# Kernel optimization log

Hardware: AMD Instinct MI355X
Metric: run time of the kernel (lower is better)

Reference implementation:

```python
import jax, jax.numpy as jnp
import numpy as np

NU = 60000   # num_users
NI = 40000   # num_items
N = NU + NI  # num_nodes
E = 2000000  # num_edges
F = 128      # feat_dim (user_feat_dim == item_feat_dim)
H = 128      # hidden_dim


def setup_inputs() -> dict:
    key = jax.random.key(0)
    ks = jax.random.split(key, 14)
    s = 0.05
    inp = {
        "x": jax.random.normal(ks[0], (N, F), jnp.float32),
        "edge_index": jax.random.randint(ks[1], (2, E), 0, N, dtype=jnp.int32),
        "node_type": jnp.concatenate([jnp.zeros(NU, jnp.int32), jnp.ones(NI, jnp.int32)]),
        # input projections (Linear stores weight as (out, in))
        "w_user": s * jax.random.normal(ks[2], (H, F), jnp.float32),
        "b_user": jnp.zeros((H,), jnp.float32),
        "w_item": s * jax.random.normal(ks[3], (H, F), jnp.float32),
        "b_item": jnp.zeros((H,), jnp.float32),
        # SAGEConv layer 0: lin_l (aggregated neighbors, with bias), lin_r (root, no bias)
        "w_l0": s * jax.random.normal(ks[4], (H, H), jnp.float32),
        "b_l0": s * jax.random.normal(ks[5], (H,), jnp.float32),
        "w_r0": s * jax.random.normal(ks[6], (H, H), jnp.float32),
        # SAGEConv layer 1
        "w_l1": s * jax.random.normal(ks[7], (H, H), jnp.float32),
        "b_l1": s * jax.random.normal(ks[8], (H,), jnp.float32),
        "w_r1": s * jax.random.normal(ks[9], (H, H), jnp.float32),
    }
    return inp


def _sage_conv(h, src, dst, w_l, b_l, w_r):
    # gather source features, max-aggregate onto destinations (PyG aggr='max')
    msg = h[src]                                          # [E, H]
    agg = jax.ops.segment_max(msg, dst, num_segments=N)   # [N, H], -inf where no in-edges
    agg = jnp.where(jnp.isneginf(agg), 0.0, agg)          # PyG fills empty segments with 0
    return agg @ w_l.T + b_l + h @ w_r.T


def reference(x, edge_index, node_type, w_user, b_user, w_item, b_item,
              w_l0, b_l0, w_r0, w_l1, b_l1, w_r1):
    # node_type is sorted: first NU rows are users, rest are items
    src, dst = edge_index[0], edge_index[1]
    user_h = x[:NU] @ w_user.T + b_user                   # [NU, H]
    item_h = x[NU:] @ w_item.T + b_item                   # [NI, H]
    h = jnp.concatenate([user_h, item_h], axis=0)         # [N, H]
    # layer 0 with residual (dims match) then ReLU; dropout is identity in eval
    h = h + _sage_conv(h, src, dst, w_l0, b_l0, w_r0)
    h = jax.nn.relu(h)
    # layer 1 with residual (no activation after last layer)
    h = h + _sage_conv(h, src, dst, w_l1, b_l1, w_r1)
    return (h[:NU], h[NU:])
```

## Files before the change

kernel.cpp:

```cpp
#include <hip/hip_runtime.h>

#define NUSR 60000
#define NITM 40000
#define NN   100000
#define EE   2000000
#define HD   128
#define NEG_BIG (-3.402823466e+38f)

#define BW   512
#define NB   196
#define EPB  8192

using bf16x8   = __attribute__((ext_vector_type(8))) short;
using f32x4    = __attribute__((ext_vector_type(4))) float;
using ushort4t = __attribute__((ext_vector_type(4))) unsigned short;

__device__ __forceinline__ unsigned short f2bf(float f) {
    unsigned int u = __float_as_uint(f);
    u += 0x7FFFu + ((u >> 16) & 1u);
    return (unsigned short)(u >> 16);
}
__device__ __forceinline__ float bf2f(unsigned short s) {
    return __uint_as_float(((unsigned int)s) << 16);
}
__device__ __forceinline__ int swz(int row, int col) {
    return row * HD + (col ^ ((row & 7) << 3));
}

__global__ __launch_bounds__(256) void bhist_k(const int* __restrict__ dst,
                                               int* __restrict__ bcnt) {
    __shared__ int h[NB];
    int t = threadIdx.x;
    if (t < NB) h[t] = 0;
    __syncthreads();
    int e0 = blockIdx.x * EPB;
    #pragma unroll 4
    for (int i = t; i < EPB; i += 256) {
        int e = e0 + i;
        if (e < EE) atomicAdd(&h[dst[e] >> 9], 1);
    }
    __syncthreads();
    if (t < NB && h[t]) atomicAdd(&bcnt[t], h[t]);
}

__global__ void bscan_k(const int* __restrict__ bcnt, int* __restrict__ bbase,
                        int* __restrict__ bcur, int* __restrict__ off) {
    __shared__ int s[256];
    int t = threadIdx.x;
    int v = (t < NB) ? bcnt[t] : 0;
    s[t] = v;
    __syncthreads();
    for (int d = 1; d < 256; d <<= 1) {
        int a = (t >= d) ? s[t - d] : 0;
        __syncthreads();
        s[t] += a;
        __syncthreads();
    }
    if (t < NB) { bbase[t] = s[t] - v; bcur[t] = s[t] - v; }
    if (t == NB - 1) { bbase[NB] = s[t]; off[NN] = EE; }
}

__global__ __launch_bounds__(256) void bscatter_k(const int* __restrict__ src,
                                                  const int* __restrict__ dst,
                                                  int* __restrict__ bcur,
                                                  uint2* __restrict__ bedge) {
    __shared__ int h[NB], base[NB];
    int t = threadIdx.x;
    if (t < NB) h[t] = 0;
    __syncthreads();
    int e0 = blockIdx.x * EPB;
    #pragma unroll 4
    for (int i = t; i < EPB; i += 256) {
        int e = e0 + i;
        if (e < EE) atomicAdd(&h[dst[e] >> 9], 1);
    }
    __syncthreads();
    if (t < NB) {
        int c = h[t];
        base[t] = c ? atomicAdd(&bcur[t], c) : 0;
        h[t] = 0;
    }
    __syncthreads();
    #pragma unroll 4
    for (int i = t; i < EPB; i += 256) {
        int e = e0 + i;
        if (e < EE) {
            int d = dst[e];
            int b = d >> 9;
            int p = base[b] + atomicAdd(&h[b], 1);
            bedge[p] = make_uint2((unsigned)src[e], (unsigned)d);
        }
    }
}

__global__ __launch_bounds__(512) void bcsr_k(const uint2* __restrict__ bedge,
                                              const int* __restrict__ bbase,
                                              int* __restrict__ off,
                                              int* __restrict__ csr) {
    __shared__ int cnt[BW], cur[BW], sc[BW];
    int b = blockIdx.x, t = threadIdx.x;
    int n0 = b * BW;
    int nloc = min(BW, NN - n0);
    cnt[t] = 0;
    __syncthreads();
    int e0 = bbase[b], e1 = bbase[b + 1];
    for (int e = e0 + t; e < e1; e += 512)
        atomicAdd(&cnt[(int)bedge[e].y - n0], 1);
    __syncthreads();
    int v = cnt[t];
    sc[t] = v;
    __syncthreads();
    for (int d = 1; d < BW; d <<= 1) {
        int a = (t >= d) ? sc[t - d] : 0;
        __syncthreads();
        sc[t] += a;
        __syncthreads();
    }
    int excl = sc[t] - v;
    if (t < nloc) { off[n0 + t] = e0 + excl; cur[t] = e0 + excl; }
    __syncthreads();
    for (int e = e0 + t; e < e1; e += 512) {
        uint2 ed = bedge[e];
        int p = atomicAdd(&cur[(int)ed.y - n0], 1);
        csr[p] = (int)ed.x;
    }
}

__global__ void cvt6_k(const float* __restrict__ a0, const float* __restrict__ a1,
                       const float* __restrict__ a2, const float* __restrict__ a3,
                       const float* __restrict__ a4, const float* __restrict__ a5,
                       unsigned short* __restrict__ out) {
    int i = blockIdx.x * 256 + threadIdx.x;
    const float* s;
    switch (i >> 14) {
        case 0: s = a0; break; case 1: s = a1; break; case 2: s = a2; break;
        case 3: s = a3; break; case 4: s = a4; break; default: s = a5; break;
    }
    out[i] = f2bf(s[i & 16383]);
}

__global__ __launch_bounds__(256) void proj_mfma_k(
    const float* __restrict__ x, const unsigned short* __restrict__ wb,
    const float* __restrict__ bias, unsigned short* __restrict__ hout,
    int row_base, int nrows) {
    __shared__ unsigned short lw[HD * HD];
    int tid = threadIdx.x;
    #pragma unroll
    for (int it = 0; it < 16; ++it) {
        int flat = (it * 256 + tid) * 4;
        int row = flat >> 7, col = flat & 127;
        *(ushort4t*)&lw[swz(row, col)] = *(const ushort4t*)(wb + flat);
    }
    __syncthreads();
    int lane = tid & 63, w = tid >> 6;
    int l15 = lane & 15, l4 = lane >> 4;
    int m0 = blockIdx.x * 128 + w * 32;
    f32x4 acc[2][8] = {};
    #pragma unroll
    for (int kb = 0; kb < 4; ++kb) {
        bf16x8 a[2];
        #pragma unroll
        for (int rt = 0; rt < 2; ++rt) {
            int r = m0 + rt * 16 + l15;
            if (r >= nrows) r = nrows - 1;
            const float* ap = x + (size_t)(row_base + r) * HD + kb * 32 + l4 * 8;
            f32x4 v0 = *(const f32x4*)ap;
            f32x4 v1 = *(const f32x4*)(ap + 4);
            bf16x8 f;
            #pragma unroll
            for (int j = 0; j < 4; ++j) { f[j] = (short)f2bf(v0[j]); f[j + 4] = (short)f2bf(v1[j]); }
            a[rt] = f;
        }
        #pragma unroll
        for (int ct = 0; ct < 8; ++ct) {
            bf16x8 b = *(const bf16x8*)&lw[swz(ct * 16 + l15, kb * 32 + l4 * 8)];
            acc[0][ct] = __builtin_amdgcn_mfma_f32_16x16x32_bf16(a[0], b, acc[0][ct], 0, 0, 0);
            acc[1][ct] = __builtin_amdgcn_mfma_f32_16x16x32_bf16(a[1], b, acc[1][ct], 0, 0, 0);
        }
    }
    #pragma unroll
    for (int ct = 0; ct < 8; ++ct) {
        int col = ct * 16 + l15;
        float bv = bias[col];
        #pragma unroll
        for (int rt = 0; rt < 2; ++rt)
            #pragma unroll
            for (int j = 0; j < 4; ++j) {
                int r = m0 + rt * 16 + l4 * 4 + j;
                if (r < nrows)
                    hout[(size_t)(row_base + r) * HD + col] = f2bf(acc[rt][ct][j] + bv);
            }
    }
}

__global__ __launch_bounds__(256) void agg_bf16_k(
    const unsigned short* __restrict__ hb, const int* __restrict__ off,
    const int* __restrict__ csr, unsigned short* __restrict__ aggb) {
    int node = (blockIdx.x * 256 + threadIdx.x) >> 6;
    int lane = threadIdx.x & 63;
    if (node >= NN) return;
    int s0 = off[node], s1 = off[node + 1];
    const unsigned int* hr = (const unsigned int*)hb;
    float m0 = NEG_BIG, m1 = NEG_BIG;
    int j = s0;
    for (; j + 3 < s1; j += 4) {
        int r0 = csr[j], r1 = csr[j + 1], r2 = csr[j + 2], r3 = csr[j + 3];
        unsigned v0 = hr[(size_t)r0 * 64 + lane];
        unsigned v1 = hr[(size_t)r1 * 64 + lane];
        unsigned v2 = hr[(size_t)r2 * 64 + lane];
        unsigned v3 = hr[(size_t)r3 * 64 + lane];
        m0 = fmaxf(fmaxf(m0, __uint_as_float(v0 << 16)), fmaxf(__uint_as_float(v1 << 16), __uint_as_float(v2 << 16)));
        m1 = fmaxf(fmaxf(m1, __uint_as_float(v0 & 0xFFFF0000u)), fmaxf(__uint_as_float(v1 & 0xFFFF0000u), __uint_as_float(v2 & 0xFFFF0000u)));
        m0 = fmaxf(m0, __uint_as_float(v3 << 16));
        m1 = fmaxf(m1, __uint_as_float(v3 & 0xFFFF0000u));
    }
    for (; j < s1; ++j) {
        unsigned v = hr[(size_t)csr[j] * 64 + lane];
        m0 = fmaxf(m0, __uint_as_float(v << 16));
        m1 = fmaxf(m1, __uint_as_float(v & 0xFFFF0000u));
    }
    unsigned outv = (s1 > s0) ? ((__float_as_uint(m0) >> 16) | (__float_as_uint(m1) & 0xFFFF0000u)) : 0u;
    ((unsigned int*)aggb)[(size_t)node * 64 + lane] = outv;
}

__global__ __launch_bounds__(256) void combine_mfma_k(
    const unsigned short* __restrict__ hb, const unsigned short* __restrict__ aggb,
    const unsigned short* __restrict__ wlb, const float* __restrict__ bl,
    const unsigned short* __restrict__ wrb,
    unsigned short* __restrict__ hnext, float* __restrict__ fout, int relu) {
    __shared__ unsigned short lw[2][HD * HD];
    int tid = threadIdx.x;
    #pragma unroll
    for (int it = 0; it < 16; ++it) {
        int flat = (it * 256 + tid) * 4;
        int row = flat >> 7, col = flat & 127;
        *(ushort4t*)&lw[0][swz(row, col)] = *(const ushort4t*)(wlb + flat);
        *(ushort4t*)&lw[1][swz(row, col)] = *(const ushort4t*)(wrb + flat);
    }
    __syncthreads();
    int lane = tid & 63, w = tid >> 6;
    int l15 = lane & 15, l4 = lane >> 4;
    int m0 = blockIdx.x * 128 + w * 32;
    f32x4 acc[2][8] = {};
    #pragma unroll
    for (int kb = 0; kb < 4; ++kb) {
        bf16x8 a1[2], a2[2];
        #pragma unroll
        for (int rt = 0; rt < 2; ++rt) {
            int r = m0 + rt * 16 + l15;
            if (r >= NN) r = NN - 1;
            size_t o = (size_t)r * HD + kb * 32 + l4 * 8;
            a1[rt] = *(const bf16x8*)(aggb + o);
            a2[rt] = *(const bf16x8*)(hb + o);
        }
        #pragma unroll
        for (int ct = 0; ct < 8; ++ct) {
            bf16x8 b1 = *(const bf16x8*)&lw[0][swz(ct * 16 + l15, kb * 32 + l4 * 8)];
            bf16x8 b2 = *(const bf16x8*)&lw[1][swz(ct * 16 + l15, kb * 32 + l4 * 8)];
            acc[0][ct] = __builtin_amdgcn_mfma_f32_16x16x32_bf16(a1[0], b1, acc[0][ct], 0, 0, 0);
            acc[0][ct] = __builtin_amdgcn_mfma_f32_16x16x32_bf16(a2[0], b2, acc[0][ct], 0, 0, 0);
            acc[1][ct] = __builtin_amdgcn_mfma_f32_16x16x32_bf16(a1[1], b1, acc[1][ct], 0, 0, 0);
            acc[1][ct] = __builtin_amdgcn_mfma_f32_16x16x32_bf16(a2[1], b2, acc[1][ct], 0, 0, 0);
        }
    }
    #pragma unroll
    for (int ct = 0; ct < 8; ++ct) {
        int col = ct * 16 + l15;
        float bv = bl[col];
        #pragma unroll
        for (int rt = 0; rt < 2; ++rt)
            #pragma unroll
            for (int j = 0; j < 4; ++j) {
                int r = m0 + rt * 16 + l4 * 4 + j;
                if (r < NN) {
                    float v = acc[rt][ct][j] + bv + bf2f(hb[(size_t)r * HD + col]);
                    if (relu) v = fmaxf(v, 0.0f);
                    if (fout) fout[(size_t)r * HD + col] = v;
                    else      hnext[(size_t)r * HD + col] = f2bf(v);
                }
            }
    }
}

extern "C" void kernel_launch(void* const* d_in, const int* in_sizes, int n_in,
                              void* d_out, int out_size, void* d_ws, size_t ws_size,
                              hipStream_t stream) {
    const float* x      = (const float*)d_in[0];
    const int*   ei     = (const int*)d_in[1];
    const float* w_user = (const float*)d_in[3];
    const float* b_user = (const float*)d_in[4];
    const float* w_item = (const float*)d_in[5];
    const float* b_item = (const float*)d_in[6];
    const float* w_l0   = (const float*)d_in[7];
    const float* b_l0   = (const float*)d_in[8];
    const float* w_r0   = (const float*)d_in[9];
    const float* w_l1   = (const float*)d_in[10];
    const float* b_l1   = (const float*)d_in[11];
    const float* w_r1   = (const float*)d_in[12];

    const int* e_src = ei;
    const int* e_dst = ei + EE;

    char* ws = (char*)d_ws;
    size_t cur_off = 0;
    auto carve = [&](size_t bytes) {
        void* p = ws + cur_off;
        cur_off = (cur_off + bytes + 255) & ~(size_t)255;
        return p;
    };
    unsigned short* hb0  = (unsigned short*)carve((size_t)NN * HD * 2);
    unsigned short* hb1  = (unsigned short*)carve((size_t)NN * HD * 2);
    unsigned short* aggb = (unsigned short*)carve((size_t)NN * HD * 2);
    unsigned short* wb   = (unsigned short*)carve((size_t)6 * HD * HD * 2);
    int*   off   = (int*)carve((size_t)(NN + 1) * 4);
    int*   csr   = (int*)carve((size_t)EE * 4);
    uint2* bedge = (uint2*)carve((size_t)EE * 8);
    int*   bcnt  = (int*)carve((NB + 1) * 4);
    int*   bbase = (int*)carve((NB + 1) * 4);
    int*   bcur  = (int*)carve((NB + 1) * 4);
    (void)ws_size;

    hipMemsetAsync(bcnt, 0, (size_t)NB * 4, stream);
    int nbB = (EE + EPB - 1) / EPB;
    bhist_k<<<nbB, 256, 0, stream>>>(e_dst, bcnt);
    bscan_k<<<1, 256, 0, stream>>>(bcnt, bbase, bcur, off);
    bscatter_k<<<nbB, 256, 0, stream>>>(e_src, e_dst, bcur, bedge);
    bcsr_k<<<NB, 512, 0, stream>>>(bedge, bbase, off, csr);

    cvt6_k<<<(6 * HD * HD) / 256, 256, 0, stream>>>(w_user, w_item, w_l0, w_r0, w_l1, w_r1, wb);

    proj_mfma_k<<<(NUSR + 127) / 128, 256, 0, stream>>>(x, wb,         b_user, hb0, 0,    NUSR);
    proj_mfma_k<<<(NITM + 127) / 128, 256, 0, stream>>>(x, wb + 16384, b_item, hb0, NUSR, NITM);

    agg_bf16_k<<<NN / 4, 256, 0, stream>>>(hb0, off, csr, aggb);
    combine_mfma_k<<<(NN + 127) / 128, 256, 0, stream>>>(
        hb0, aggb, wb + 2 * 16384, b_l0, wb + 3 * 16384, hb1, nullptr, 1);

    agg_bf16_k<<<NN / 4, 256, 0, stream>>>(hb1, off, csr, aggb);
    combine_mfma_k<<<(NN + 127) / 128, 256, 0, stream>>>(
        hb1, aggb, wb + 4 * 16384, b_l1, wb + 5 * 16384, nullptr, (float*)d_out, 0);
}
```

Measured before the change: 355.5 us.

## Aggregate max over order-preserving uint16 keys and pack bucketed edges into 32 bits

The projection and combine kernels now also write an order-preserving unsigned 16-bit key copy of each bf16 feature. The max aggregation then uses packed u16 vector max over 8 unrolled neighbors with wave-uniform indices, and decodes the key back to bf16 once at the end. Bucketed edges are packed into one 32-bit word (local dst in the high bits, src in the low 17 bits) instead of uint2, which halves that intermediate traffic. The cost is an extra 25.6 MB key write per layer and one more workspace buffer.

```diff
diff --git a/kernel.cpp b/kernel.cpp
--- a/kernel.cpp
+++ b/kernel.cpp
@@ -5,7 +5,6 @@
 #define NN   100000
 #define EE   2000000
 #define HD   128
-#define NEG_BIG (-3.402823466e+38f)
 
 #define BW   512
 #define NB   196
@@ -14,6 +13,7 @@
 using bf16x8   = __attribute__((ext_vector_type(8))) short;
 using f32x4    = __attribute__((ext_vector_type(4))) float;
 using ushort4t = __attribute__((ext_vector_type(4))) unsigned short;
+using ushort2t = __attribute__((ext_vector_type(2))) unsigned short;
 
 __device__ __forceinline__ unsigned short f2bf(float f) {
     unsigned int u = __float_as_uint(f);
@@ -22,6 +22,9 @@
 }
 __device__ __forceinline__ float bf2f(unsigned short s) {
     return __uint_as_float(((unsigned int)s) << 16);
+}
+__device__ __forceinline__ unsigned short keyof(unsigned short b) {
+    return (b & 0x8000u) ? (unsigned short)~b : (unsigned short)(b | 0x8000u);
 }
 __device__ __forceinline__ int swz(int row, int col) {
     return row * HD + (col ^ ((row & 7) << 3));
@@ -63,7 +66,7 @@
 __global__ __launch_bounds__(256) void bscatter_k(const int* __restrict__ src,
                                                   const int* __restrict__ dst,
                                                   int* __restrict__ bcur,
-                                                  uint2* __restrict__ bedge) {
+                                                  unsigned int* __restrict__ bedge) {
     __shared__ int h[NB], base[NB];
     int t = threadIdx.x;
     if (t < NB) h[t] = 0;
@@ -88,12 +91,12 @@
             int d = dst[e];
             int b = d >> 9;
             int p = base[b] + atomicAdd(&h[b], 1);
-            bedge[p] = make_uint2((unsigned)src[e], (unsigned)d);
-        }
-    }
-}
-
-__global__ __launch_bounds__(512) void bcsr_k(const uint2* __restrict__ bedge,
+            bedge[p] = ((unsigned)(d - (b << 9)) << 17) | (unsigned)src[e];
+        }
+    }
+}
+
+__global__ __launch_bounds__(512) void bcsr_k(const unsigned int* __restrict__ bedge,
                                               const int* __restrict__ bbase,
                                               int* __restrict__ off,
                                               int* __restrict__ csr) {
@@ -105,7 +108,7 @@
     __syncthreads();
     int e0 = bbase[b], e1 = bbase[b + 1];
     for (int e = e0 + t; e < e1; e += 512)
-        atomicAdd(&cnt[(int)bedge[e].y - n0], 1);
+        atomicAdd(&cnt[bedge[e] >> 17], 1);
     __syncthreads();
     int v = cnt[t];
     sc[t] = v;
@@ -120,9 +123,9 @@
     if (t < nloc) { off[n0 + t] = e0 + excl; cur[t] = e0 + excl; }
     __syncthreads();
     for (int e = e0 + t; e < e1; e += 512) {
-        uint2 ed = bedge[e];
-        int p = atomicAdd(&cur[(int)ed.y - n0], 1);
-        csr[p] = (int)ed.x;
+        unsigned ed = bedge[e];
+        int p = atomicAdd(&cur[ed >> 17], 1);
+        csr[p] = (int)(ed & 0x1FFFFu);
     }
 }
 
@@ -142,7 +145,7 @@
 __global__ __launch_bounds__(256) void proj_mfma_k(
     const float* __restrict__ x, const unsigned short* __restrict__ wb,
     const float* __restrict__ bias, unsigned short* __restrict__ hout,
-    int row_base, int nrows) {
+    unsigned short* __restrict__ hkey, int row_base, int nrows) {
     __shared__ unsigned short lw[HD * HD];
     int tid = threadIdx.x;
     #pragma unroll
@@ -187,47 +190,57 @@
             #pragma unroll
             for (int j = 0; j < 4; ++j) {
                 int r = m0 + rt * 16 + l4 * 4 + j;
-                if (r < nrows)
-                    hout[(size_t)(row_base + r) * HD + col] = f2bf(acc[rt][ct][j] + bv);
+                if (r < nrows) {
+                    unsigned short b16 = f2bf(acc[rt][ct][j] + bv);
+                    size_t o = (size_t)(row_base + r) * HD + col;
+                    hout[o] = b16;
+                    hkey[o] = keyof(b16);
+                }
             }
     }
 }
 
-__global__ __launch_bounds__(256) void agg_bf16_k(
-    const unsigned short* __restrict__ hb, const int* __restrict__ off,
-    const int* __restrict__ csr, unsigned short* __restrict__ aggb) {
+__global__ __launch_bounds__(256) void agg_key_k(
+    const unsigned int* __restrict__ hkey, const int* __restrict__ off,
+    const int* __restrict__ csr, unsigned int* __restrict__ aggb) {
     int node = (blockIdx.x * 256 + threadIdx.x) >> 6;
     int lane = threadIdx.x & 63;
     if (node >= NN) return;
     int s0 = off[node], s1 = off[node + 1];
-    const unsigned int* hr = (const unsigned int*)hb;
-    float m0 = NEG_BIG, m1 = NEG_BIG;
+    ushort2t m = {0, 0};
     int j = s0;
-    for (; j + 3 < s1; j += 4) {
-        int r0 = csr[j], r1 = csr[j + 1], r2 = csr[j + 2], r3 = csr[j + 3];
-        unsigned v0 = hr[(size_t)r0 * 64 + lane];
-        unsigned v1 = hr[(size_t)r1 * 64 + lane];
-        unsigned v2 = hr[(size_t)r2 * 64 + lane];
-        unsigned v3 = hr[(size_t)r3 * 64 + lane];
-        m0 = fmaxf(fmaxf(m0, __uint_as_float(v0 << 16)), fmaxf(__uint_as_float(v1 << 16), __uint_as_float(v2 << 16)));
-        m1 = fmaxf(fmaxf(m1, __uint_as_float(v0 & 0xFFFF0000u)), fmaxf(__uint_as_float(v1 & 0xFFFF0000u), __uint_as_float(v2 & 0xFFFF0000u)));
-        m0 = fmaxf(m0, __uint_as_float(v3 << 16));
-        m1 = fmaxf(m1, __uint_as_float(v3 & 0xFFFF0000u));
+    for (; j + 7 < s1; j += 8) {
+        ushort2t v[8];
+        #pragma unroll
+        for (int u = 0; u < 8; ++u) {
+            int r = __builtin_amdgcn_readfirstlane(csr[j + u]);
+            unsigned w = hkey[(size_t)r * 64 + lane];
+            v[u] = *(ushort2t*)&w;
+        }
+        #pragma unroll
+        for (int u = 0; u < 4; ++u) v[u] = __builtin_elementwise_max(v[u], v[u + 4]);
+        v[0] = __builtin_elementwise_max(v[0], v[2]);
+        v[1] = __builtin_elementwise_max(v[1], v[3]);
+        v[0] = __builtin_elementwise_max(v[0], v[1]);
+        m = __builtin_elementwise_max(m, v[0]);
     }
     for (; j < s1; ++j) {
-        unsigned v = hr[(size_t)csr[j] * 64 + lane];
-        m0 = fmaxf(m0, __uint_as_float(v << 16));
-        m1 = fmaxf(m1, __uint_as_float(v & 0xFFFF0000u));
-    }
-    unsigned outv = (s1 > s0) ? ((__float_as_uint(m0) >> 16) | (__float_as_uint(m1) & 0xFFFF0000u)) : 0u;
-    ((unsigned int*)aggb)[(size_t)node * 64 + lane] = outv;
+        int r = __builtin_amdgcn_readfirstlane(csr[j]);
+        unsigned w = hkey[(size_t)r * 64 + lane];
+        m = __builtin_elementwise_max(m, *(ushort2t*)&w);
+    }
+    unsigned k = *(unsigned*)&m;
+    unsigned negsel = (~k & 0x80008000u) >> 15;
+    unsigned x = k ^ (0x80008000u | (negsel * 0x7FFFu));
+    ((unsigned int*)aggb)[(size_t)node * 64 + lane] = (s1 > s0) ? x : 0u;
 }
 
 __global__ __launch_bounds__(256) void combine_mfma_k(
     const unsigned short* __restrict__ hb, const unsigned short* __restrict__ aggb,
     const unsigned short* __restrict__ wlb, const float* __restrict__ bl,
     const unsigned short* __restrict__ wrb,
-    unsigned short* __restrict__ hnext, float* __restrict__ fout, int relu) {
+    unsigned short* __restrict__ hnext, unsigned short* __restrict__ hkey,
+    float* __restrict__ fout, int relu) {
     __shared__ unsigned short lw[2][HD * HD];
     int tid = threadIdx.x;
     #pragma unroll
@@ -275,8 +288,14 @@
                 if (r < NN) {
                     float v = acc[rt][ct][j] + bv + bf2f(hb[(size_t)r * HD + col]);
                     if (relu) v = fmaxf(v, 0.0f);
-                    if (fout) fout[(size_t)r * HD + col] = v;
-                    else      hnext[(size_t)r * HD + col] = f2bf(v);
+                    size_t o = (size_t)r * HD + col;
+                    if (fout) {
+                        fout[o] = v;
+                    } else {
+                        unsigned short b16 = f2bf(v);
+                        hnext[o] = b16;
+                        hkey[o] = keyof(b16);
+                    }
                 }
             }
     }
@@ -311,13 +330,14 @@
     unsigned short* hb0  = (unsigned short*)carve((size_t)NN * HD * 2);
     unsigned short* hb1  = (unsigned short*)carve((size_t)NN * HD * 2);
     unsigned short* aggb = (unsigned short*)carve((size_t)NN * HD * 2);
+    unsigned short* hkey = (unsigned short*)carve((size_t)NN * HD * 2);
     unsigned short* wb   = (unsigned short*)carve((size_t)6 * HD * HD * 2);
-    int*   off   = (int*)carve((size_t)(NN + 1) * 4);
-    int*   csr   = (int*)carve((size_t)EE * 4);
-    uint2* bedge = (uint2*)carve((size_t)EE * 8);
-    int*   bcnt  = (int*)carve((NB + 1) * 4);
-    int*   bbase = (int*)carve((NB + 1) * 4);
-    int*   bcur  = (int*)carve((NB + 1) * 4);
+    int*      off   = (int*)carve((size_t)(NN + 1) * 4);
+    int*      csr   = (int*)carve((size_t)EE * 4);
+    unsigned* bedge = (unsigned*)carve((size_t)EE * 4);
+    int*      bcnt  = (int*)carve((NB + 1) * 4);
+    int*      bbase = (int*)carve((NB + 1) * 4);
+    int*      bcur  = (int*)carve((NB + 1) * 4);
     (void)ws_size;
 
     hipMemsetAsync(bcnt, 0, (size_t)NB * 4, stream);
@@ -329,14 +349,14 @@
 
     cvt6_k<<<(6 * HD * HD) / 256, 256, 0, stream>>>(w_user, w_item, w_l0, w_r0, w_l1, w_r1, wb);
 
-    proj_mfma_k<<<(NUSR + 127) / 128, 256, 0, stream>>>(x, wb,         b_user, hb0, 0,    NUSR);
-    proj_mfma_k<<<(NITM + 127) / 128, 256, 0, stream>>>(x, wb + 16384, b_item, hb0, NUSR, NITM);
-
-    agg_bf16_k<<<NN / 4, 256, 0, stream>>>(hb0, off, csr, aggb);
+    proj_mfma_k<<<(NUSR + 127) / 128, 256, 0, stream>>>(x, wb,         b_user, hb0, hkey, 0,    NUSR);
+    proj_mfma_k<<<(NITM + 127) / 128, 256, 0, stream>>>(x, wb + 16384, b_item, hb0, hkey, NUSR, NITM);
+
+    agg_key_k<<<NN / 4, 256, 0, stream>>>((const unsigned*)hkey, off, csr, (unsigned*)aggb);
     combine_mfma_k<<<(NN + 127) / 128, 256, 0, stream>>>(
-        hb0, aggb, wb + 2 * 16384, b_l0, wb + 3 * 16384, hb1, nullptr, 1);
-
-    agg_bf16_k<<<NN / 4, 256, 0, stream>>>(hb1, off, csr, aggb);
+        hb0, aggb, wb + 2 * 16384, b_l0, wb + 3 * 16384, hb1, hkey, nullptr, 1);
+
+    agg_key_k<<<NN / 4, 256, 0, stream>>>((const unsigned*)hkey, off, csr, (unsigned*)aggb);
     combine_mfma_k<<<(NN + 127) / 128, 256, 0, stream>>>(
-        hb1, aggb, wb + 4 * 16384, b_l1, wb + 5 * 16384, nullptr, (float*)d_out, 0);
-}
+        hb1, aggb, wb + 4 * 16384, b_l1, wb + 5 * 16384, nullptr, nullptr, (float*)d_out, 0);
+}
```

New measurement: 368.0 us. 1.03x slower.
